# Optimization experiments

Hardware: AMD Instinct MI355X
Metric: run time of the kernel (lower is better)

## Reference

```python
import jax, jax.numpy as jnp
import numpy as np

RANK = 8
LN_EPS = 1e-5


def setup_inputs() -> dict:
    key = jax.random.key(0)
    ks = jax.random.split(key, 8)
    B, T, D = 16, 1024, 1024
    A = 1024          # ada_dim
    I = 1024          # inter_dim
    OUT = D * RANK * 4  # 32768
    s = 0.02
    return {
        "x": jax.random.normal(ks[0], (B, T, D), jnp.float32),
        "ada_emb": jax.random.normal(ks[1], (B, A), jnp.float32),
        "base_up": jax.random.normal(ks[2], (D, D), jnp.float32) * s,
        "base_down": jax.random.normal(ks[3], (D, D), jnp.float32) * s,
        "ln_gamma": jnp.ones((A,), jnp.float32),
        "ln_beta": jnp.zeros((A,), jnp.float32),
        "W1": jax.random.normal(ks[4], (A, I), jnp.float32) / np.sqrt(A),
        "bias1": jnp.zeros((I,), jnp.float32),
        "W2": jax.random.normal(ks[5], (I, OUT), jnp.float32) / np.sqrt(I),
        "bias2": jnp.zeros((OUT,), jnp.float32),
    }


def reference(x, ada_emb, base_up, base_down, ln_gamma, ln_beta, W1, bias1, W2, bias2):
    B, T, D = x.shape
    R = RANK
    # norm_cond: LayerNorm over ada_dim (biased variance, eps=1e-5)
    mu = jnp.mean(ada_emb, axis=-1, keepdims=True)
    var = jnp.mean(jnp.square(ada_emb - mu), axis=-1, keepdims=True)
    c = (ada_emb - mu) / jnp.sqrt(var + LN_EPS) * ln_gamma + ln_beta
    # gen_weight: Linear -> GELU -> Linear
    h = jax.nn.gelu(c @ W1 + bias1, approximate=False)
    w = h @ W2 + bias2                         # (B, 4*D*R)
    a1, b1, a2, b2 = [t.reshape(B, D, R) for t in jnp.split(w, 4, axis=-1)]
    # down matvec: x @ (base_down + a2 @ b2^T), factored to avoid (B,D,D)
    u = jnp.einsum('btd,bdr->btr', x, a2)      # (B,T,R)
    mid = jnp.einsum('btd,dl->btl', x, base_down) + jnp.einsum('btr,blr->btl', u, b2)
    mid = jax.nn.gelu(mid, approximate=False)  # act_fn between layers
    # up matvec: (base_up + a1 @ b1^T) @ mid, factored
    v = jnp.einsum('blr,btl->btr', b1, mid)    # (B,T,R)
    out = jnp.einsum('btl,kl->btk', mid, base_up) + jnp.einsum('bkr,btr->btk', a1, v)
    return x + out  # residual
```

## Files before the change

### kernel.cpp

```cpp
#include <hip/hip_runtime.h>
#include <math.h>

#define DD 1024
#define NB 16
#define WSPLIT 32
#define HSPLIT 32

typedef unsigned short u16;
typedef __attribute__((ext_vector_type(8))) short short8;
typedef __attribute__((ext_vector_type(4))) float f32x4;
typedef __attribute__((ext_vector_type(16))) float f32x16;

__device__ __forceinline__ float gelu_f(float x) {
  return 0.5f * x * (1.0f + erff(x * 0.70710678118654752440f));
}
__device__ __forceinline__ u16 f2bf(float f) {
  union { float f; unsigned u; } v; v.f = f;
  return (u16)((v.u + 0x7FFFu + ((v.u >> 16) & 1u)) >> 16);
}
__device__ __forceinline__ float bf2f(u16 b) {
  union { unsigned u; float f; } v; v.u = ((unsigned)b) << 16;
  return v.f;
}
__device__ __forceinline__ void gload_lds16(const u16* g, u16* l) {
  __builtin_amdgcn_global_load_lds(
      (const __attribute__((address_space(1))) void*)g,
      (__attribute__((address_space(3))) void*)l, 16, 0, 0);
}

#define VMCNT8   asm volatile("s_waitcnt vmcnt(8)" ::: "memory")
#define VMCNT0   asm volatile("s_waitcnt vmcnt(0)" ::: "memory")
#define BARRIER  asm volatile("s_barrier" ::: "memory")

__launch_bounds__(256)
__global__ void prep_kernel(const float* __restrict__ x, u16* __restrict__ xb,
                            const float* __restrict__ ada, const float* __restrict__ gamma,
                            const float* __restrict__ beta, float* __restrict__ c,
                            const float* __restrict__ bdn, u16* __restrict__ bdTb,
                            const float* __restrict__ bu, u16* __restrict__ bub) {
  __shared__ float smem[1056];
  int bid = blockIdx.x;
  int t = threadIdx.x;
  if (bid < 8192) {
    size_t i = (size_t)bid * 256 + t;
    const float4* xf = (const float4*)x;
    float4 v0 = xf[i * 2], v1 = xf[i * 2 + 1];
    short8 o;
    o[0] = (short)f2bf(v0.x); o[1] = (short)f2bf(v0.y);
    o[2] = (short)f2bf(v0.z); o[3] = (short)f2bf(v0.w);
    o[4] = (short)f2bf(v1.x); o[5] = (short)f2bf(v1.y);
    o[6] = (short)f2bf(v1.z); o[7] = (short)f2bf(v1.w);
    *(short8*)(xb + i * 8) = o;
  } else if (bid < 8208) {
    int b = bid - 8192;
    const float* row = ada + b * DD;
    float s = 0.f, s2 = 0.f;
    for (int i = t; i < DD; i += 256) { float v = row[i]; s += v; s2 += v * v; }
    for (int off = 32; off; off >>= 1) { s += __shfl_down(s, off); s2 += __shfl_down(s2, off); }
    float* rs = smem; float* rs2 = smem + 4;
    int wave = t >> 6, lane = t & 63;
    if (lane == 0) { rs[wave] = s; rs2[wave] = s2; }
    __syncthreads();
    if (t == 0) {
      float a = 0.f, a2 = 0.f;
      for (int w = 0; w < 4; w++) { a += rs[w]; a2 += rs2[w]; }
      rs[0] = a * (1.0f / DD); rs2[0] = a2 * (1.0f / DD);
    }
    __syncthreads();
    float mu = rs[0];
    float var = rs2[0] - mu * mu;
    float inv = rsqrtf(var + 1e-5f);
    for (int i = t; i < DD; i += 256)
      c[b * DD + i] = (row[i] - mu) * inv * gamma[i] + beta[i];
  } else if (bid < 9232) {
    int t2 = bid - 8208;
    int bx = (t2 & 31) * 32, by = (t2 >> 5) * 32;
    float (*tile)[33] = (float(*)[33])smem;
    int tx = t & 31, ty = t >> 5;
    for (int r = ty; r < 32; r += 8) tile[r][tx] = bdn[(size_t)(by + r) * DD + bx + tx];
    __syncthreads();
    for (int r = ty; r < 32; r += 8)
      bdTb[(size_t)(bx + r) * DD + by + tx] = f2bf(tile[tx][r]);
  } else {
    size_t i = (size_t)(bid - 9232) * 256 + t;
    const float4* bf = (const float4*)bu;
    float4 v0 = bf[i * 2], v1 = bf[i * 2 + 1];
    short8 o;
    o[0] = (short)f2bf(v0.x); o[1] = (short)f2bf(v0.y);
    o[2] = (short)f2bf(v0.z); o[3] = (short)f2bf(v0.w);
    o[4] = (short)f2bf(v1.x); o[5] = (short)f2bf(v1.y);
    o[6] = (short)f2bf(v1.z); o[7] = (short)f2bf(v1.w);
    *(short8*)(bub + i * 8) = o;
  }
}

__launch_bounds__(256)
__global__ void h_part_kernel(const float* __restrict__ c, const float* __restrict__ W1,
                              float* __restrict__ hpart) {
  int s = blockIdx.y;
  int j = blockIdx.x * 256 + threadIdx.x;
  int k0 = s * 32;
  __shared__ float cs[NB][32];
  for (int i = threadIdx.x; i < NB * 32; i += 256)
    cs[i >> 5][i & 31] = c[(size_t)(i >> 5) * DD + k0 + (i & 31)];
  __syncthreads();
  float acc[NB];
  #pragma unroll
  for (int b = 0; b < NB; b++) acc[b] = 0.f;
  #pragma unroll
  for (int al = 0; al < 32; al++) {
    float wv = W1[(size_t)(k0 + al) * DD + j];
    #pragma unroll
    for (int b = 0; b < NB; b++) acc[b] += cs[b][al] * wv;
  }
  #pragma unroll
  for (int b = 0; b < NB; b++)
    hpart[((size_t)s * NB + b) * DD + j] = acc[b];
}

__launch_bounds__(256)
__global__ void w_part_kernel(const float* __restrict__ hpart, const float* __restrict__ bias1,
                              const float* __restrict__ W2, float* __restrict__ part) {
  int s = blockIdx.y;
  int j4 = blockIdx.x * 256 + threadIdx.x;
  int k0 = s * 32;
  int t = threadIdx.x;
  __shared__ float hl[NB][32];
  #pragma unroll
  for (int v = 0; v < 2; v++) {
    int i = t + v * 256;
    int b = i >> 5, kk = i & 31;
    float acc = bias1[k0 + kk];
    #pragma unroll 8
    for (int ss = 0; ss < HSPLIT; ss++) acc += hpart[((size_t)ss * NB + b) * DD + k0 + kk];
    hl[b][kk] = gelu_f(acc);
  }
  __syncthreads();
  f32x4 acc[NB];
  #pragma unroll
  for (int b = 0; b < NB; b++) acc[b] = f32x4{0.f, 0.f, 0.f, 0.f};
  const float4* W2v = (const float4*)W2;
  #pragma unroll 8
  for (int al = 0; al < 32; al++) {
    float4 wv = W2v[(size_t)(k0 + al) * 8192 + j4];
    #pragma unroll
    for (int b = 0; b < NB; b++) {
      float hb = hl[b][al];
      acc[b][0] += hb * wv.x; acc[b][1] += hb * wv.y;
      acc[b][2] += hb * wv.z; acc[b][3] += hb * wv.w;
    }
  }
  f32x4* pv = (f32x4*)part;
  #pragma unroll
  for (int b = 0; b < NB; b++)
    pv[((size_t)s * NB + b) * 8192 + j4] = acc[b];
}

__launch_bounds__(256)
__global__ void w_reduce_kernel(const float* __restrict__ part, const float* __restrict__ bias2,
                                float* __restrict__ w) {
  int idx = blockIdx.x * 256 + threadIdx.x;
  int j = idx & 32767;
  float acc = bias2[j];
  #pragma unroll
  for (int s = 0; s < WSPLIT; s++) acc += part[(size_t)s * NB * 32768 + idx];
  w[idx] = acc;
}

__launch_bounds__(256)
__global__ void pack_lora_kernel(const u16* __restrict__ src, const float* __restrict__ w,
                                 int aoff, int boff,
                                 u16* __restrict__ aext, u16* __restrict__ bext) {
  int b = blockIdx.y;
  const float* wb = w + (size_t)b * 32768;
  int t = threadIdx.x;
  short8 z = {};
  if (blockIdx.x < 16) {
    __shared__ float a2s[8192];
    for (int i = t; i < 8192; i += 256) a2s[i] = wb[aoff + i];
    __syncthreads();
    int row = blockIdx.x * 64 + (t >> 2);
    int q = t & 3;
    const u16* xr = src + ((size_t)b << 20) + (size_t)row * DD + q * 256;
    float acc[8] = {};
    #pragma unroll 4
    for (int kk = 0; kk < 32; kk++) {
      short8 xv = *(const short8*)(xr + kk * 8);
      #pragma unroll
      for (int e = 0; e < 8; e++) {
        float xf = bf2f((u16)xv[e]);
        int d = q * 256 + kk * 8 + e;
        #pragma unroll
        for (int r = 0; r < 8; r++) acc[r] += xf * a2s[d * 8 + r];
      }
    }
    #pragma unroll
    for (int r = 0; r < 8; r++) {
      acc[r] += __shfl_xor(acc[r], 1);
      acc[r] += __shfl_xor(acc[r], 2);
    }
    short8 ov = z;
    if (q == 0) {
      #pragma unroll
      for (int r = 0; r < 8; r++) ov[r] = (short)f2bf(acc[r]);
    }
    u16* orow = aext + ((size_t)b * 1024 + row) * 64 + q * 16;
    *(short8*)orow = ov;
    *(short8*)(orow + 8) = z;
  } else {
    for (int l = t; l < 1024; l += 256) {
      short8 ov;
      #pragma unroll
      for (int r = 0; r < 8; r++) ov[r] = (short)f2bf(wb[boff + l * 8 + r]);
      u16* orow = bext + ((size_t)b * 1024 + l) * 64;
      *(short8*)orow = ov;
      #pragma unroll
      for (int k = 1; k < 8; k++) *(short8*)(orow + k * 8) = z;
    }
  }
}

#define STAGE_A(KT, BUF) do { int kt_ = (KT);                                          \
    if (kt_ < 16) { int ks_ = kt_ * 64;                                                \
      _Pragma("unroll")                                                                \
      for (int c_ = 0; c_ < 4; c_++)                                                   \
        gload_lds16(Ab + (size_t)srow[c_] * DD + ks_ + se[c_], As[BUF] + ldsel[c_]);   \
    } else {                                                                           \
      _Pragma("unroll")                                                                \
      for (int c_ = 0; c_ < 4; c_++)                                                   \
        gload_lds16(Ae + (size_t)srow[c_] * 64 + se[c_], As[BUF] + ldsel[c_]);         \
    } } while (0)
#define STAGE_B(KT, BUF) do { int kt_ = (KT);                                          \
    if (kt_ < 16) { int ks_ = kt_ * 64;                                                \
      _Pragma("unroll")                                                                \
      for (int c_ = 0; c_ < 4; c_++)                                                   \
        gload_lds16(Bb + (size_t)srow[c_] * DD + ks_ + se[c_], Bs[BUF] + ldsel[c_]);   \
    } else {                                                                           \
      _Pragma("unroll")                                                                \
      for (int c_ = 0; c_ < 4; c_++)                                                   \
        gload_lds16(Be + (size_t)srow[c_] * 64 + se[c_], Bs[BUF] + ldsel[c_]);         \
    } } while (0)

template<int PHASE>
__launch_bounds__(512, 2)
__global__ void gemm256_kernel(const u16* __restrict__ A, const u16* __restrict__ BT,
                               const u16* __restrict__ Aext, const u16* __restrict__ Bext,
                               const u16* __restrict__ resid, void* __restrict__ Cout) {
  constexpr int BK = 64;
  constexpr int NT = 17;
  __shared__ __align__(16) u16 As[2][256 * BK];
  __shared__ __align__(16) u16 Bs[2][256 * BK];

  int orig = blockIdx.x;
  int logical = (orig & 7) * 32 + (orig >> 3);
  int b = logical >> 4;
  int tile = logical & 15;
  int tm = tile >> 2, tn = tile & 3;

  const u16* Ab = A + ((size_t)b << 20) + (size_t)(tm * 256) * DD;
  const u16* Bb = BT + (size_t)(tn * 256) * DD;
  const u16* Ae = Aext + ((size_t)b * 1024 + tm * 256) * 64;
  const u16* Be = Bext + ((size_t)b * 1024 + tn * 256) * 64;

  int t = threadIdx.x, lane = t & 63;
  int l31 = lane & 31, kb = (lane >> 5) * 8;
  int wave = t >> 6;
  int wm = wave >> 2, wn = wave & 3;

  int srow[4], se[4], ldsel[4];
  #pragma unroll
  for (int c = 0; c < 4; c++) {
    int chunk = c * 512 + t;
    srow[c] = chunk >> 3;
    se[c] = ((chunk & 7) ^ (srow[c] & 7)) << 3;
    ldsel[c] = chunk * 8;
  }

  f32x16 acc[4][2] = {};

  STAGE_A(0, 0); STAGE_B(0, 0);
  STAGE_A(1, 1); STAGE_B(1, 1);
  VMCNT8;
  BARRIER;

  int cur = 0;
  #pragma unroll 1
  for (int kt = 0; kt < NT; kt++) {
    const u16* Ap = As[cur];
    const u16* Bp = Bs[cur];
    short8 afr[2][4], bf0[4], bf1[4];

    #pragma unroll
    for (int ks = 0; ks < 4; ks++) {
      #pragma unroll
      for (int rt = 0; rt < 2; rt++) {
        int r = wm * 128 + rt * 32 + l31;
        int e = (ks * 16 + kb) ^ ((r & 7) << 3);
        afr[rt][ks] = *(const short8*)(Ap + r * BK + e);
      }
      {
        int r = wn * 64 + l31;
        int e = (ks * 16 + kb) ^ ((r & 7) << 3);
        bf0[ks] = *(const short8*)(Bp + r * BK + e);
      }
    }
    BARRIER;
    __builtin_amdgcn_s_setprio(1);
    #pragma unroll
    for (int ks = 0; ks < 4; ks++)
      #pragma unroll
      for (int rt = 0; rt < 2; rt++)
        acc[rt][0] = __builtin_amdgcn_mfma_f32_32x32x16_bf16(afr[rt][ks], bf0[ks], acc[rt][0], 0, 0, 0);
    __builtin_amdgcn_s_setprio(0);
    BARRIER;

    #pragma unroll
    for (int ks = 0; ks < 4; ks++) {
      int r = wn * 64 + 32 + l31;
      int e = (ks * 16 + kb) ^ ((r & 7) << 3);
      bf1[ks] = *(const short8*)(Bp + r * BK + e);
    }
    BARRIER;
    __builtin_amdgcn_s_setprio(1);
    #pragma unroll
    for (int ks = 0; ks < 4; ks++)
      #pragma unroll
      for (int rt = 0; rt < 2; rt++)
        acc[rt][1] = __builtin_amdgcn_mfma_f32_32x32x16_bf16(afr[rt][ks], bf1[ks], acc[rt][1], 0, 0, 0);
    __builtin_amdgcn_s_setprio(0);
    BARRIER;

    if (kt + 2 < NT) STAGE_B(kt + 2, cur);
    #pragma unroll
    for (int ks = 0; ks < 4; ks++)
      #pragma unroll
      for (int rt = 0; rt < 2; rt++) {
        int r = wm * 128 + (rt + 2) * 32 + l31;
        int e = (ks * 16 + kb) ^ ((r & 7) << 3);
        afr[rt][ks] = *(const short8*)(Ap + r * BK + e);
      }
    BARRIER;
    __builtin_amdgcn_s_setprio(1);
    #pragma unroll
    for (int ks = 0; ks < 4; ks++)
      #pragma unroll
      for (int rt = 0; rt < 2; rt++)
        acc[rt + 2][1] = __builtin_amdgcn_mfma_f32_32x32x16_bf16(afr[rt][ks], bf1[ks], acc[rt + 2][1], 0, 0, 0);
    __builtin_amdgcn_s_setprio(0);
    BARRIER;

    if (kt + 2 < NT) STAGE_A(kt + 2, cur);
    __builtin_amdgcn_s_setprio(1);
    #pragma unroll
    for (int ks = 0; ks < 4; ks++)
      #pragma unroll
      for (int rt = 0; rt < 2; rt++)
        acc[rt + 2][0] = __builtin_amdgcn_mfma_f32_32x32x16_bf16(afr[rt][ks], bf0[ks], acc[rt + 2][0], 0, 0, 0);
    __builtin_amdgcn_s_setprio(0);
    if (kt + 2 < NT) { VMCNT8; } else { VMCNT0; }
    BARRIER;

    cur ^= 1;
  }

  int r0 = tm * 256 + wm * 128 + (lane >> 5) * 4;
  int c0 = tn * 256 + wn * 64 + l31;
  if (PHASE == 1) {
    u16* mid = (u16*)Cout + ((size_t)b << 20);
    #pragma unroll
    for (int rt = 0; rt < 4; rt++)
      #pragma unroll
      for (int ct = 0; ct < 2; ct++)
        #pragma unroll
        for (int reg = 0; reg < 16; reg++) {
          int row = r0 + rt * 32 + (reg & 3) + 8 * (reg >> 2);
          int col = c0 + ct * 32;
          mid[(size_t)row * DD + col] = f2bf(gelu_f(acc[rt][ct][reg]));
        }
  } else {
    float* out = (float*)Cout + ((size_t)b << 20);
    const u16* xb = resid + ((size_t)b << 20);
    #pragma unroll
    for (int rt = 0; rt < 4; rt++)
      #pragma unroll
      for (int ct = 0; ct < 2; ct++)
        #pragma unroll
        for (int reg = 0; reg < 16; reg++) {
          int row = r0 + rt * 32 + (reg & 3) + 8 * (reg >> 2);
          int col = c0 + ct * 32;
          size_t idx = (size_t)row * DD + col;
          out[idx] = bf2f(xb[idx]) + acc[rt][ct][reg];
        }
  }
}

extern "C" void kernel_launch(void* const* d_in, const int* in_sizes, int n_in,
                              void* d_out, int out_size, void* d_ws, size_t ws_size,
                              hipStream_t stream) {
  const float* x         = (const float*)d_in[0];
  const float* ada       = (const float*)d_in[1];
  const float* base_up   = (const float*)d_in[2];
  const float* base_down = (const float*)d_in[3];
  const float* gamma     = (const float*)d_in[4];
  const float* beta      = (const float*)d_in[5];
  const float* W1        = (const float*)d_in[6];
  const float* bias1     = (const float*)d_in[7];
  const float* W2        = (const float*)d_in[8];
  const float* bias2     = (const float*)d_in[9];
  float* out = (float*)d_out;
  char* ws = (char*)d_ws;

  float* c     = (float*)(ws);
  float* w     = (float*)(ws + 0x20000);
  u16*   bdTb  = (u16*)  (ws + 0x220000);
  u16*   bub   = (u16*)  (ws + 0x420000);
  float* hpart = (float*)(ws + 0x620000);
  u16*   xb    = (u16*)  (ws + 0x820000);
  u16*   uext  = (u16*)  (ws + 0x2820000);
  u16*   b2ext = (u16*)  (ws + 0x2A20000);
  u16*   vext  = (u16*)  (ws + 0x2C20000);
  u16*   a1ext = (u16*)  (ws + 0x2E20000);
  u16*   mid   = (u16*)  (ws + 0x3020000);
  float* part  = (float*)(ws + 0x5020000);

  prep_kernel<<<dim3(9744), dim3(256), 0, stream>>>(x, xb, ada, gamma, beta, c,
                                                    base_down, bdTb, base_up, bub);
  h_part_kernel<<<dim3(4, HSPLIT), dim3(256), 0, stream>>>(c, W1, hpart);
  w_part_kernel<<<dim3(32, WSPLIT), dim3(256), 0, stream>>>(hpart, bias1, W2, part);
  w_reduce_kernel<<<dim3(2048), dim3(256), 0, stream>>>(part, bias2, w);
  pack_lora_kernel<<<dim3(17, 16), dim3(256), 0, stream>>>(xb, w, 16384, 24576, uext, b2ext);
  gemm256_kernel<1><<<dim3(256), dim3(512), 0, stream>>>(xb, bdTb, uext, b2ext,
                                                         (const u16*)nullptr, (void*)mid);
  pack_lora_kernel<<<dim3(17, 16), dim3(256), 0, stream>>>(mid, w, 8192, 0, vext, a1ext);
  gemm256_kernel<2><<<dim3(256), dim3(512), 0, stream>>>(mid, bub, vext, a1ext, xb, (void*)out);
}
```

Baseline: 284.1 us.

## Pipeline W2 loads through LDS double buffer and hoist h reduction into separate kernel

Moves the reduction of h partials, bias add and GELU out of w_part_kernel into a new h_reduce_kernel, so the work is done once rather than redundantly by every block. w_part_kernel now streams W2 rows into a double-buffered LDS tile with global_load_lds, using explicit waitcnt and barriers, and handles 64 k-rows per block. WSPLIT is halved, which halves the partial buffer that w_reduce_kernel must read. The cost is an extra kernel launch and fewer blocks in flight for the W2 pass.

```diff
diff --git a/kernel.cpp b/kernel.cpp
--- a/kernel.cpp
+++ b/kernel.cpp
@@ -3,7 +3,7 @@
 
 #define DD 1024
 #define NB 16
-#define WSPLIT 32
+#define WSPLIT 16
 #define HSPLIT 32
 
 typedef unsigned short u16;
@@ -23,6 +23,11 @@
   return v.f;
 }
 __device__ __forceinline__ void gload_lds16(const u16* g, u16* l) {
+  __builtin_amdgcn_global_load_lds(
+      (const __attribute__((address_space(1))) void*)g,
+      (__attribute__((address_space(3))) void*)l, 16, 0, 0);
+}
+__device__ __forceinline__ void gload_lds16f(const float* g, float* l) {
   __builtin_amdgcn_global_load_lds(
       (const __attribute__((address_space(1))) void*)g,
       (__attribute__((address_space(3))) void*)l, 16, 0, 0);
@@ -119,37 +124,82 @@
 }
 
 __launch_bounds__(256)
-__global__ void w_part_kernel(const float* __restrict__ hpart, const float* __restrict__ bias1,
-                              const float* __restrict__ W2, float* __restrict__ part) {
+__global__ void h_reduce_kernel(const float* __restrict__ hpart, const float* __restrict__ bias1,
+                                float* __restrict__ h) {
+  int idx = blockIdx.x * 256 + threadIdx.x;
+  int j = idx & (DD - 1);
+  float acc = bias1[j];
+  #pragma unroll
+  for (int s = 0; s < HSPLIT; s++) acc += hpart[(size_t)s * NB * DD + idx];
+  h[idx] = gelu_f(acc);
+}
+
+#define WSTAGE(I8, BUF) do { int kr_ = k0 + (I8) * 8;                                \
+    _Pragma("unroll")                                                                \
+    for (int r_ = 0; r_ < 8; r_++)                                                   \
+      gload_lds16f(W2 + (size_t)(kr_ + r_) * 32768 + j0 + t4, &wlds[BUF][r_][t4]);   \
+  } while (0)
+
+__launch_bounds__(256)
+__global__ void w_part_kernel(const float* __restrict__ h, const float* __restrict__ W2,
+                              float* __restrict__ part) {
   int s = blockIdx.y;
-  int j4 = blockIdx.x * 256 + threadIdx.x;
-  int k0 = s * 32;
+  int j0 = blockIdx.x * 1024;
+  int k0 = s * 64;
   int t = threadIdx.x;
-  __shared__ float hl[NB][32];
-  #pragma unroll
-  for (int v = 0; v < 2; v++) {
+  int t4 = t * 4;
+  __shared__ __align__(16) float wlds[2][8][1024];
+  __shared__ __align__(16) float hlT[64][16];
+
+  float hv[4];
+  #pragma unroll
+  for (int v = 0; v < 4; v++) {
     int i = t + v * 256;
-    int b = i >> 5, kk = i & 31;
-    float acc = bias1[k0 + kk];
-    #pragma unroll 8
-    for (int ss = 0; ss < HSPLIT; ss++) acc += hpart[((size_t)ss * NB + b) * DD + k0 + kk];
-    hl[b][kk] = gelu_f(acc);
-  }
-  __syncthreads();
+    hv[v] = h[(size_t)(i & 15) * DD + k0 + (i >> 4)];
+  }
+  #pragma unroll
+  for (int v = 0; v < 4; v++) {
+    int i = t + v * 256;
+    hlT[i >> 4][i & 15] = hv[v];
+  }
+
+  WSTAGE(0, 0);
+  WSTAGE(1, 1);
+
   f32x4 acc[NB];
   #pragma unroll
   for (int b = 0; b < NB; b++) acc[b] = f32x4{0.f, 0.f, 0.f, 0.f};
-  const float4* W2v = (const float4*)W2;
-  #pragma unroll 8
-  for (int al = 0; al < 32; al++) {
-    float4 wv = W2v[(size_t)(k0 + al) * 8192 + j4];
-    #pragma unroll
-    for (int b = 0; b < NB; b++) {
-      float hb = hl[b][al];
-      acc[b][0] += hb * wv.x; acc[b][1] += hb * wv.y;
-      acc[b][2] += hb * wv.z; acc[b][3] += hb * wv.w;
-    }
-  }
+
+  #pragma unroll 1
+  for (int i8 = 0; i8 < 8; i8++) {
+    if (i8 < 7) { VMCNT8; } else { VMCNT0; }
+    BARRIER;
+    int buf = i8 & 1;
+    #pragma unroll
+    for (int r = 0; r < 8; r++) {
+      f32x4 wv = *(const f32x4*)&wlds[buf][r][t4];
+      int kk = i8 * 8 + r;
+      f32x4 hx0 = *(const f32x4*)&hlT[kk][0];
+      f32x4 hx1 = *(const f32x4*)&hlT[kk][4];
+      f32x4 hx2 = *(const f32x4*)&hlT[kk][8];
+      f32x4 hx3 = *(const f32x4*)&hlT[kk][12];
+      #pragma unroll
+      for (int q = 0; q < 4; q++) {
+        acc[q][0] += hx0[q] * wv[0]; acc[q][1] += hx0[q] * wv[1];
+        acc[q][2] += hx0[q] * wv[2]; acc[q][3] += hx0[q] * wv[3];
+        acc[q + 4][0] += hx1[q] * wv[0]; acc[q + 4][1] += hx1[q] * wv[1];
+        acc[q + 4][2] += hx1[q] * wv[2]; acc[q + 4][3] += hx1[q] * wv[3];
+        acc[q + 8][0] += hx2[q] * wv[0]; acc[q + 8][1] += hx2[q] * wv[1];
+        acc[q + 8][2] += hx2[q] * wv[2]; acc[q + 8][3] += hx2[q] * wv[3];
+        acc[q + 12][0] += hx3[q] * wv[0]; acc[q + 12][1] += hx3[q] * wv[1];
+        acc[q + 12][2] += hx3[q] * wv[2]; acc[q + 12][3] += hx3[q] * wv[3];
+      }
+    }
+    BARRIER;
+    if (i8 + 2 < 8) WSTAGE(i8 + 2, buf);
+  }
+
+  int j4 = blockIdx.x * 256 + t;
   f32x4* pv = (f32x4*)part;
   #pragma unroll
   for (int b = 0; b < NB; b++)
@@ -411,6 +461,7 @@
   char* ws = (char*)d_ws;
 
   float* c     = (float*)(ws);
+  float* h     = (float*)(ws + 0x10000);
   float* w     = (float*)(ws + 0x20000);
   u16*   bdTb  = (u16*)  (ws + 0x220000);
   u16*   bub   = (u16*)  (ws + 0x420000);
@@ -426,7 +477,8 @@
   prep_kernel<<<dim3(9744), dim3(256), 0, stream>>>(x, xb, ada, gamma, beta, c,
                                                     base_down, bdTb, base_up, bub);
   h_part_kernel<<<dim3(4, HSPLIT), dim3(256), 0, stream>>>(c, W1, hpart);
-  w_part_kernel<<<dim3(32, WSPLIT), dim3(256), 0, stream>>>(hpart, bias1, W2, part);
+  h_reduce_kernel<<<dim3(64), dim3(256), 0, stream>>>(hpart, bias1, h);
+  w_part_kernel<<<dim3(32, WSPLIT), dim3(256), 0, stream>>>(h, W2, part);
   w_reduce_kernel<<<dim3(2048), dim3(256), 0, stream>>>(part, bias2, w);
   pack_lora_kernel<<<dim3(17, 16), dim3(256), 0, stream>>>(xb, w, 16384, 24576, uext, b2ext);
   gemm256_kernel<1><<<dim3(256), dim3(512), 0, stream>>>(xb, bdTb, uext, b2ext,
```

New measurement: 258.1 us. -9.1%, faster.
